# Kernel optimization log

Measured on AMD Instinct MI355X. Metric: run time of the kernel, lower is better.

## Reference

```python
import jax, jax.numpy as jnp
import numpy as np

N_NODES = 100000


def _gcn_layer(h_in, W, b, src, dst, n_nodes):
    """PyG GCNConv: out = D^{-1/2} (A + I) D^{-1/2} (h_in @ W) + b.
    src/dst already include self-loops. Messages flow src -> dst."""
    h = h_in @ W  # [N, C_out]
    ones = jnp.ones(dst.shape[0], dtype=h.dtype)
    deg = jax.ops.segment_sum(ones, dst, num_segments=n_nodes)  # in-degree incl. self-loops
    dinv = jnp.where(deg > 0, jax.lax.rsqrt(deg), 0.0)
    norm = dinv[src] * dinv[dst]  # [E]
    msg = norm[:, None] * h[src]  # gather + scale, [E, C_out]
    out = jax.ops.segment_sum(msg, dst, num_segments=n_nodes)
    return out + b


def setup_inputs() -> dict:
    key = jax.random.key(0)
    ks = jax.random.split(key, 4)
    d_in, d_hid = 64, 64
    n_edges = 1600000
    x = jax.random.normal(ks[0], (N_NODES, d_in), dtype=jnp.float32)
    edge_index = jax.random.randint(ks[1], (2, n_edges), 0, N_NODES, dtype=jnp.int64)
    W1 = jax.random.normal(ks[2], (d_in, d_hid), dtype=jnp.float32) * (1.0 / np.sqrt(d_in))
    b1 = jnp.zeros((d_hid,), dtype=jnp.float32)
    W2 = jax.random.normal(ks[3], (d_hid, d_hid), dtype=jnp.float32) * (1.0 / np.sqrt(d_hid))
    b2 = jnp.zeros((d_hid,), dtype=jnp.float32)
    return {"x": x, "edge_index": edge_index, "W1": W1, "b1": b1, "W2": W2, "b2": b2}


def reference(x, edge_index, W1, b1, W2, b2):
    n = x.shape[0]
    loop = jnp.arange(n, dtype=edge_index.dtype)
    src = jnp.concatenate([edge_index[0], loop])  # add self-loops once, reused by both layers
    dst = jnp.concatenate([edge_index[1], loop])
    h = jax.nn.relu(_gcn_layer(x, W1, b1, src, dst, n))
    h = jax.nn.relu(_gcn_layer(h, W2, b2, src, dst, n))
    return h
```

## Files before the change

kernel.cpp:

```cpp
#include <hip/hip_runtime.h>
#include <hip/hip_bf16.h>


#define NDIM 64
#define BSHIFT 9
#define BNODES (1 << BSHIFT)
#define BCAP 10240
#define CHUNK 4096
#define PHASES 13
#define PSHIFT 13

typedef float v2f __attribute__((ext_vector_type(2)));
typedef __attribute__((ext_vector_type(8))) short short8b;
typedef __attribute__((ext_vector_type(4))) float f32x4;

__device__ __forceinline__ unsigned f2bf_rne(float f) {
  unsigned u = __float_as_uint(f);
  return (u + 0x7fffu + ((u >> 16) & 1u)) >> 16;
}

__global__ void init_cursor_kernel(int* __restrict__ bcursor, int nbuck) {
  int b = blockIdx.x * 256 + threadIdx.x;
  if (b < nbuck) bcursor[b] = b * BCAP;
}

__global__ __launch_bounds__(256) void bin_scatter_kernel(
    const int* __restrict__ src, const int* __restrict__ dst,
    int* __restrict__ bcursor, unsigned* __restrict__ binned, int nedges) {
  __shared__ int lcnt[256], lbase[256], lcur[256], gbase[256], tscan[256];
  __shared__ int2 stage[CHUNK];
  int t = threadIdx.x;
  int i0 = blockIdx.x * CHUNK;
  int iend = i0 + CHUNK; if (iend > nedges) iend = nedges;
  lcnt[t] = 0;
  __syncthreads();
  for (int i = i0 + t; i < iend; i += 256)
    atomicAdd(&lcnt[dst[i] >> BSHIFT], 1);
  __syncthreads();
  tscan[t] = lcnt[t];
  __syncthreads();
  for (int off = 1; off < 256; off <<= 1) {
    int tv = (t >= off) ? tscan[t - off] : 0;
    __syncthreads();
    tscan[t] += tv;
    __syncthreads();
  }
  lbase[t] = tscan[t] - lcnt[t];
  lcur[t] = lbase[t];
  if (lcnt[t] > 0) gbase[t] = atomicAdd(&bcursor[t], lcnt[t]);
  __syncthreads();
  for (int i = i0 + t; i < iend; i += 256) {
    int s = src[i], d = dst[i];
    int p = atomicAdd(&lcur[d >> BSHIFT], 1);
    stage[p] = make_int2(s, d);
  }
  __syncthreads();
  int cnt = iend - i0;
  for (int i = t; i < cnt; i += 256) {
    int2 pr = stage[i];
    int b = pr.y >> BSHIFT;
    unsigned pk = (((unsigned)(pr.y & (BNODES - 1))) << 17) | (unsigned)pr.x;
    int idx = gbase[b] + (i - lbase[b]);
    if (idx < (b + 1) * BCAP) binned[idx] = pk;
  }
}

__global__ __launch_bounds__(256) void csr_build_kernel(
    const unsigned* __restrict__ binned, const int* __restrict__ bcursor,
    int* __restrict__ rowbeg, int* __restrict__ rowend,
    int* __restrict__ csr_src, float* __restrict__ dinv, int n) {
  __shared__ int deg[BNODES], rpl[BNODES], tscan[256];
  __shared__ int pcnt[BNODES * PHASES];
  int b = blockIdx.x, t = threadIdx.x;
  int node0 = b << BSHIFT;
  int ncnt = n - node0; if (ncnt > BNODES) ncnt = BNODES;
  int e0 = b * BCAP;
  int ecnt = bcursor[b] - e0;
  if (ecnt > BCAP) ecnt = BCAP;
  for (int i = t; i < BNODES * PHASES; i += 256) pcnt[i] = 0;
  __syncthreads();
  for (int i = t; i < ecnt; i += 256) {
    unsigned u = binned[e0 + i];
    atomicAdd(&pcnt[(u >> 17) * PHASES + ((u & 0x1FFFFu) >> PSHIFT)], 1);
  }
  __syncthreads();
  for (int i = t; i < BNODES; i += 256) {
    int s = 0;
#pragma unroll
    for (int p = 0; p < PHASES; ++p) {
      int c = pcnt[i * PHASES + p];
      pcnt[i * PHASES + p] = s;
      s += c;
    }
    deg[i] = s;
  }
  __syncthreads();
  int d0 = deg[2 * t], d1 = deg[2 * t + 1];
  int ps = d0 + d1;
  tscan[t] = ps;
  __syncthreads();
  for (int off = 1; off < 256; off <<= 1) {
    int tv = (t >= off) ? tscan[t - off] : 0;
    __syncthreads();
    tscan[t] += tv;
    __syncthreads();
  }
  int eb = tscan[t] - ps;
  rpl[2 * t] = eb;
  rpl[2 * t + 1] = eb + d0;
  __syncthreads();
  for (int i = t; i < ncnt; i += 256) {
    rowbeg[node0 + i] = e0 + rpl[i];
    rowend[node0 + i] = e0 + rpl[i] + deg[i];
    dinv[node0 + i] = rsqrtf((float)deg[i] + 1.0f);
  }
  __syncthreads();
  for (int i = t; i < ecnt; i += 256) {
    unsigned u = binned[e0 + i];
    int nd = u >> 17;
    int s = (int)(u & 0x1FFFFu);
    int pos = rpl[nd] + atomicAdd(&pcnt[nd * PHASES + (s >> PSHIFT)], 1);
    csr_src[e0 + pos] = s;
  }
}

template <bool BF16IN>
__global__ __launch_bounds__(256) void gemm_mfma_kernel(
    const void* __restrict__ Xin, const float* __restrict__ W,
    const float* __restrict__ dinv, ushort* __restrict__ hsb, int nrows) {
  __shared__ __attribute__((aligned(16))) ushort stage[4][16 * NDIM];
  const int tid = threadIdx.x;
  const int l = tid & 63;
  const int wv = tid >> 6;
  const int lrow = l & 15;
  const int kg = l >> 4;

  short8b Whi[4][2], Wlo[4][2];
#pragma unroll
  for (int ct = 0; ct < 4; ++ct) {
#pragma unroll
    for (int ks = 0; ks < 2; ++ks) {
      const int c = ct * 16 + lrow;
      const int k0 = ks * 32 + kg * 8;
#pragma unroll
      for (int i = 0; i < 8; ++i) {
        float w = W[(k0 + i) * NDIM + c];
        unsigned hb = f2bf_rne(w);
        float hf = __uint_as_float(hb << 16);
        Whi[ct][ks][i] = (short)hb;
        Wlo[ct][ks][i] = (short)f2bf_rne(w - hf);
      }
    }
  }

  const int tiles = (nrows + 15) >> 4;
  for (int tb = blockIdx.x * 4; tb < tiles; tb += gridDim.x * 4) {
    const int t = tb + wv;
    const int row0 = t << 4;
    const int r = row0 + lrow;
    short8b Ahi[2], Alo[2];
    if (BF16IN) {
      const uint4* Xb = (const uint4*)Xin;
#pragma unroll
      for (int ks = 0; ks < 2; ++ks) {
        uint4 q = make_uint4(0u, 0u, 0u, 0u);
        if (r < nrows) q = Xb[(size_t)r * 8 + ks * 4 + kg];
        union { uint4 u; short8b s; } cv; cv.u = q;
        Ahi[ks] = cv.s;
        Alo[ks] = cv.s;
      }
    } else {
      const float4* Xf = (const float4*)Xin;
#pragma unroll
      for (int ks = 0; ks < 2; ++ks) {
        float4 xa = make_float4(0.f, 0.f, 0.f, 0.f);
        float4 xb = make_float4(0.f, 0.f, 0.f, 0.f);
        if (r < nrows) {
          xa = Xf[(size_t)r * 16 + ks * 8 + kg * 2];
          xb = Xf[(size_t)r * 16 + ks * 8 + kg * 2 + 1];
        }
        float xs[8] = {xa.x, xa.y, xa.z, xa.w, xb.x, xb.y, xb.z, xb.w};
#pragma unroll
        for (int i = 0; i < 8; ++i) {
          unsigned hb = f2bf_rne(xs[i]);
          float hf = __uint_as_float(hb << 16);
          Ahi[ks][i] = (short)hb;
          Alo[ks][i] = (short)f2bf_rne(xs[i] - hf);
        }
      }
    }
    f32x4 acc[4];
#pragma unroll
    for (int ct = 0; ct < 4; ++ct) {
      f32x4 a = {0.f, 0.f, 0.f, 0.f};
#pragma unroll
      for (int ks = 0; ks < 2; ++ks) {
        a = __builtin_amdgcn_mfma_f32_16x16x32_bf16(Ahi[ks], Whi[ct][ks], a, 0, 0, 0);
        a = __builtin_amdgcn_mfma_f32_16x16x32_bf16(Ahi[ks], Wlo[ct][ks], a, 0, 0, 0);
        if (!BF16IN)
          a = __builtin_amdgcn_mfma_f32_16x16x32_bf16(Alo[ks], Whi[ct][ks], a, 0, 0, 0);
      }
      acc[ct] = a;
    }
#pragma unroll
    for (int q = 0; q < 4; ++q) {
      const int rr = row0 + kg * 4 + q;
      const float di = (rr < nrows) ? dinv[rr] : 0.f;
#pragma unroll
      for (int ct = 0; ct < 4; ++ct)
        stage[wv][(kg * 4 + q) * NDIM + ct * 16 + lrow] =
            (ushort)f2bf_rne(acc[ct][q] * di);
    }
    __syncthreads();
#pragma unroll
    for (int e = 0; e < 2; ++e) {
      const int idx = e * 64 + l;
      const int rw = idx >> 3;
      if (row0 + rw < nrows)
        ((uint4*)hsb)[(size_t)(row0 + rw) * 8 + (idx & 7)] =
            ((const uint4*)stage[wv])[idx];
    }
    __syncthreads();
  }
}

__device__ __forceinline__ void add8(v2f* acc, uint4 q) {
  v2f a0, a1, a2, a3;
  a0.x = __uint_as_float(q.x << 16); a0.y = __uint_as_float(q.x & 0xffff0000u);
  a1.x = __uint_as_float(q.y << 16); a1.y = __uint_as_float(q.y & 0xffff0000u);
  a2.x = __uint_as_float(q.z << 16); a2.y = __uint_as_float(q.z & 0xffff0000u);
  a3.x = __uint_as_float(q.w << 16); a3.y = __uint_as_float(q.w & 0xffff0000u);
  acc[0] += a0; acc[1] += a1; acc[2] += a2; acc[3] += a3;
}

template <bool BF16OUT>
__global__ __launch_bounds__(256) void agg_epi_kernel(
    const int* __restrict__ rowbeg, const int* __restrict__ rowend,
    const int* __restrict__ csr_src, const uint4* __restrict__ hsb4,
    const float* __restrict__ dinv, const float4* __restrict__ b4,
    void* __restrict__ outp, int n) {
  int node = blockIdx.x * 4 + (threadIdx.x >> 6);
  if (node >= n) return;
  int l = threadIdx.x & 63;
  int sub = l >> 3, g = l & 7;
  int beg = rowbeg[node], end = rowend[node];
  v2f acc[4];
#pragma unroll
  for (int i = 0; i < 4; ++i) acc[i] = (v2f)(0.f);
  for (int base = beg; base < end; base += 64) {
    int m = end - base; if (m > 64) m = 64;
    int sidx = (l < m) ? csr_src[base + l] : 0;
    int j = 0;
    for (; j + 16 <= m; j += 16) {
      int s0 = __shfl(sidx, j + sub);
      int s1 = __shfl(sidx, j + 8 + sub);
      uint4 q0 = hsb4[(size_t)s0 * 8 + g];
      uint4 q1 = hsb4[(size_t)s1 * 8 + g];
      add8(acc, q0);
      add8(acc, q1);
    }
    for (; j < m; j += 8) {
      int e = j + sub;
      int s = __shfl(sidx, e < m ? e : 0);
      uint4 q = hsb4[(size_t)s * 8 + g];
      if (e < m) add8(acc, q);
    }
  }
  if (sub == 0) add8(acc, hsb4[(size_t)node * 8 + g]);
  float a[8];
#pragma unroll
  for (int i = 0; i < 4; ++i) { a[2 * i] = acc[i].x; a[2 * i + 1] = acc[i].y; }
#pragma unroll
  for (int i = 0; i < 8; ++i) {
    a[i] += __shfl_xor(a[i], 8);
    a[i] += __shfl_xor(a[i], 16);
    a[i] += __shfl_xor(a[i], 32);
  }
  if (sub == 0) {
    float di = dinv[node];
    float4 bb0 = b4[2 * g], bb1 = b4[2 * g + 1];
    float o[8];
    o[0] = fmaxf(di * a[0] + bb0.x, 0.f);
    o[1] = fmaxf(di * a[1] + bb0.y, 0.f);
    o[2] = fmaxf(di * a[2] + bb0.z, 0.f);
    o[3] = fmaxf(di * a[3] + bb0.w, 0.f);
    o[4] = fmaxf(di * a[4] + bb1.x, 0.f);
    o[5] = fmaxf(di * a[5] + bb1.y, 0.f);
    o[6] = fmaxf(di * a[6] + bb1.z, 0.f);
    o[7] = fmaxf(di * a[7] + bb1.w, 0.f);
    if (BF16OUT) {
      uint4 wv;
      wv.x = f2bf_rne(o[0]) | (f2bf_rne(o[1]) << 16);
      wv.y = f2bf_rne(o[2]) | (f2bf_rne(o[3]) << 16);
      wv.z = f2bf_rne(o[4]) | (f2bf_rne(o[5]) << 16);
      wv.w = f2bf_rne(o[6]) | (f2bf_rne(o[7]) << 16);
      ((uint4*)outp)[(size_t)node * 8 + g] = wv;
    } else {
      float4 o0 = make_float4(o[0], o[1], o[2], o[3]);
      float4 o1 = make_float4(o[4], o[5], o[6], o[7]);
      ((float4*)outp)[(size_t)node * 16 + 2 * g] = o0;
      ((float4*)outp)[(size_t)node * 16 + 2 * g + 1] = o1;
    }
  }
}

extern "C" void kernel_launch(void* const* d_in, const int* in_sizes, int n_in,
                              void* d_out, int out_size, void* d_ws, size_t ws_size,
                              hipStream_t stream) {
  const float* x  = (const float*)d_in[0];
  const int* eidx = (const int*)d_in[1];
  const float* W1 = (const float*)d_in[2];
  const float* b1 = (const float*)d_in[3];
  const float* W2 = (const float*)d_in[4];
  const float* b2 = (const float*)d_in[5];
  float* out = (float*)d_out;

  const int N = in_sizes[0] / NDIM;
  const int E = in_sizes[1] / 2;
  const int* src = eidx;
  const int* dst = eidx + E;
  const int NV = N * NDIM;
  const int nbuck = (N + BNODES - 1) >> BSHIFT;
  const int nchunk = (E + CHUNK - 1) / CHUNK;

  auto al128 = [](size_t v) { return (v + 127) & ~(size_t)127; };
  char* w = (char*)d_ws;
  unsigned* binned = (unsigned*)w;  w += al128((size_t)nbuck * BCAP * 4);
  int*   csr_src = (int*)w;    w += al128((size_t)nbuck * BCAP * 4);
  int*   rowbeg  = (int*)w;    w += al128((size_t)N * 4);
  int*   rowend  = (int*)w;    w += al128((size_t)N * 4);
  float* dinv    = (float*)w;  w += al128((size_t)N * 4);
  int*   bcursor = (int*)w;    w += 2048;
  ushort* hsb = (ushort*)w;  w += al128((size_t)NV * 2);
  ushort* h2b = (ushort*)w;

  init_cursor_kernel<<<1, 256, 0, stream>>>(bcursor, nbuck);
  bin_scatter_kernel<<<nchunk, 256, 0, stream>>>(src, dst, bcursor, binned, E);
  csr_build_kernel<<<nbuck, 256, 0, stream>>>(binned, bcursor, rowbeg, rowend,
                                              csr_src, dinv, N);

  gemm_mfma_kernel<false><<<512, 256, 0, stream>>>(x, W1, dinv, hsb, N);
  agg_epi_kernel<true><<<(N + 3) / 4, 256, 0, stream>>>(
      rowbeg, rowend, csr_src, (const uint4*)hsb, dinv, (const float4*)b1, h2b, N);

  gemm_mfma_kernel<true><<<512, 256, 0, stream>>>(h2b, W2, dinv, hsb, N);
  agg_epi_kernel<false><<<(N + 3) / 4, 256, 0, stream>>>(
      rowbeg, rowend, csr_src, (const uint4*)hsb, dinv, (const float4*)b2, out, N);
}
```

Before: 245.8 us.

## Fuse all GCN stages into one persistent cooperative kernel with grid syncs

The seven separate launches (cursor init, binning, CSR build, two GEMMs, two aggregations) become a single cooperative persistent kernel. Each stage is a grid-stride device function, and grid.sync() separates the stages. Shared memory is a union of the per-stage layouts, and CHUNK is reduced to keep the LDS footprint low enough for 4 blocks per CU. This removes launch gaps and tail effects between kernels. In exchange, every stage runs at a fixed occupancy, register pressure is shared across all phases, and grid-wide barriers carry their own cost.

Measured after the change: 746.1 us. +203.5%, slower.

```diff
diff --git a/kernel.cpp b/kernel.cpp
--- a/kernel.cpp
+++ b/kernel.cpp
@@ -1,12 +1,15 @@
 #include <hip/hip_runtime.h>
+#include <hip/hip_cooperative_groups.h>
 #include <hip/hip_bf16.h>
+
+namespace cg = cooperative_groups;
 
 
 #define NDIM 64
 #define BSHIFT 9
 #define BNODES (1 << BSHIFT)
 #define BCAP 10240
-#define CHUNK 4096
+#define CHUNK 3072
 #define PHASES 13
 #define PSHIFT 13
 
@@ -14,121 +17,132 @@
 typedef __attribute__((ext_vector_type(8))) short short8b;
 typedef __attribute__((ext_vector_type(4))) float f32x4;
 
+struct BinSh {
+  int lcnt[256], lbase[256], lcur[256], gbase[256], tscan[256];
+  int2 stage[CHUNK];
+};
+struct CsrSh {
+  int deg[BNODES], rpl[BNODES], tscan[256];
+  int pcnt[BNODES * PHASES];
+};
+union SharedU {
+  BinSh bin;
+  CsrSh csr;
+  ushort gstage[4][16 * NDIM];
+};
+
 __device__ __forceinline__ unsigned f2bf_rne(float f) {
   unsigned u = __float_as_uint(f);
   return (u + 0x7fffu + ((u >> 16) & 1u)) >> 16;
 }
 
-__global__ void init_cursor_kernel(int* __restrict__ bcursor, int nbuck) {
-  int b = blockIdx.x * 256 + threadIdx.x;
-  if (b < nbuck) bcursor[b] = b * BCAP;
-}
-
-__global__ __launch_bounds__(256) void bin_scatter_kernel(
-    const int* __restrict__ src, const int* __restrict__ dst,
-    int* __restrict__ bcursor, unsigned* __restrict__ binned, int nedges) {
-  __shared__ int lcnt[256], lbase[256], lcur[256], gbase[256], tscan[256];
-  __shared__ int2 stage[CHUNK];
-  int t = threadIdx.x;
-  int i0 = blockIdx.x * CHUNK;
-  int iend = i0 + CHUNK; if (iend > nedges) iend = nedges;
-  lcnt[t] = 0;
-  __syncthreads();
-  for (int i = i0 + t; i < iend; i += 256)
-    atomicAdd(&lcnt[dst[i] >> BSHIFT], 1);
-  __syncthreads();
-  tscan[t] = lcnt[t];
-  __syncthreads();
-  for (int off = 1; off < 256; off <<= 1) {
-    int tv = (t >= off) ? tscan[t - off] : 0;
-    __syncthreads();
-    tscan[t] += tv;
-    __syncthreads();
-  }
-  lbase[t] = tscan[t] - lcnt[t];
-  lcur[t] = lbase[t];
-  if (lcnt[t] > 0) gbase[t] = atomicAdd(&bcursor[t], lcnt[t]);
-  __syncthreads();
-  for (int i = i0 + t; i < iend; i += 256) {
-    int s = src[i], d = dst[i];
-    int p = atomicAdd(&lcur[d >> BSHIFT], 1);
-    stage[p] = make_int2(s, d);
-  }
-  __syncthreads();
-  int cnt = iend - i0;
-  for (int i = t; i < cnt; i += 256) {
-    int2 pr = stage[i];
-    int b = pr.y >> BSHIFT;
-    unsigned pk = (((unsigned)(pr.y & (BNODES - 1))) << 17) | (unsigned)pr.x;
-    int idx = gbase[b] + (i - lbase[b]);
-    if (idx < (b + 1) * BCAP) binned[idx] = pk;
-  }
-}
-
-__global__ __launch_bounds__(256) void csr_build_kernel(
-    const unsigned* __restrict__ binned, const int* __restrict__ bcursor,
-    int* __restrict__ rowbeg, int* __restrict__ rowend,
-    int* __restrict__ csr_src, float* __restrict__ dinv, int n) {
-  __shared__ int deg[BNODES], rpl[BNODES], tscan[256];
-  __shared__ int pcnt[BNODES * PHASES];
-  int b = blockIdx.x, t = threadIdx.x;
-  int node0 = b << BSHIFT;
-  int ncnt = n - node0; if (ncnt > BNODES) ncnt = BNODES;
-  int e0 = b * BCAP;
-  int ecnt = bcursor[b] - e0;
-  if (ecnt > BCAP) ecnt = BCAP;
-  for (int i = t; i < BNODES * PHASES; i += 256) pcnt[i] = 0;
-  __syncthreads();
-  for (int i = t; i < ecnt; i += 256) {
-    unsigned u = binned[e0 + i];
-    atomicAdd(&pcnt[(u >> 17) * PHASES + ((u & 0x1FFFFu) >> PSHIFT)], 1);
-  }
-  __syncthreads();
-  for (int i = t; i < BNODES; i += 256) {
-    int s = 0;
-#pragma unroll
-    for (int p = 0; p < PHASES; ++p) {
-      int c = pcnt[i * PHASES + p];
-      pcnt[i * PHASES + p] = s;
-      s += c;
-    }
-    deg[i] = s;
-  }
-  __syncthreads();
-  int d0 = deg[2 * t], d1 = deg[2 * t + 1];
-  int ps = d0 + d1;
-  tscan[t] = ps;
-  __syncthreads();
-  for (int off = 1; off < 256; off <<= 1) {
-    int tv = (t >= off) ? tscan[t - off] : 0;
-    __syncthreads();
-    tscan[t] += tv;
-    __syncthreads();
-  }
-  int eb = tscan[t] - ps;
-  rpl[2 * t] = eb;
-  rpl[2 * t + 1] = eb + d0;
-  __syncthreads();
-  for (int i = t; i < ncnt; i += 256) {
-    rowbeg[node0 + i] = e0 + rpl[i];
-    rowend[node0 + i] = e0 + rpl[i] + deg[i];
-    dinv[node0 + i] = rsqrtf((float)deg[i] + 1.0f);
-  }
-  __syncthreads();
-  for (int i = t; i < ecnt; i += 256) {
-    unsigned u = binned[e0 + i];
-    int nd = u >> 17;
-    int s = (int)(u & 0x1FFFFu);
-    int pos = rpl[nd] + atomicAdd(&pcnt[nd * PHASES + (s >> PSHIFT)], 1);
-    csr_src[e0 + pos] = s;
+__device__ void phase_bin(const int* __restrict__ src, const int* __restrict__ dst,
+                          int* __restrict__ bcursor, unsigned* __restrict__ binned,
+                          int nedges, int nchunk, SharedU& sh) {
+  const int t = threadIdx.x;
+  for (int c = blockIdx.x; c < nchunk; c += gridDim.x) {
+    int i0 = c * CHUNK;
+    int iend = i0 + CHUNK; if (iend > nedges) iend = nedges;
+    sh.bin.lcnt[t] = 0;
+    __syncthreads();
+    for (int i = i0 + t; i < iend; i += 256)
+      atomicAdd(&sh.bin.lcnt[dst[i] >> BSHIFT], 1);
+    __syncthreads();
+    sh.bin.tscan[t] = sh.bin.lcnt[t];
+    __syncthreads();
+    for (int off = 1; off < 256; off <<= 1) {
+      int tv = (t >= off) ? sh.bin.tscan[t - off] : 0;
+      __syncthreads();
+      sh.bin.tscan[t] += tv;
+      __syncthreads();
+    }
+    sh.bin.lbase[t] = sh.bin.tscan[t] - sh.bin.lcnt[t];
+    sh.bin.lcur[t] = sh.bin.lbase[t];
+    if (sh.bin.lcnt[t] > 0) sh.bin.gbase[t] = atomicAdd(&bcursor[t], sh.bin.lcnt[t]);
+    __syncthreads();
+    for (int i = i0 + t; i < iend; i += 256) {
+      int s = src[i], d = dst[i];
+      int p = atomicAdd(&sh.bin.lcur[d >> BSHIFT], 1);
+      sh.bin.stage[p] = make_int2(s, d);
+    }
+    __syncthreads();
+    int cnt = iend - i0;
+    for (int i = t; i < cnt; i += 256) {
+      int2 pr = sh.bin.stage[i];
+      int b = pr.y >> BSHIFT;
+      unsigned pk = (((unsigned)(pr.y & (BNODES - 1))) << 17) | (unsigned)pr.x;
+      int idx = sh.bin.gbase[b] + (i - sh.bin.lbase[b]);
+      if (idx < (b + 1) * BCAP) binned[idx] = pk;
+    }
+    __syncthreads();
+  }
+}
+
+__device__ void phase_csr(const unsigned* __restrict__ binned,
+                          const int* __restrict__ bcursor,
+                          int* __restrict__ rowbeg, int* __restrict__ rowend,
+                          int* __restrict__ csr_src, float* __restrict__ dinv,
+                          int n, int nbuck, SharedU& sh) {
+  const int t = threadIdx.x;
+  for (int b = blockIdx.x; b < nbuck; b += gridDim.x) {
+    int node0 = b << BSHIFT;
+    int ncnt = n - node0; if (ncnt > BNODES) ncnt = BNODES;
+    int e0 = b * BCAP;
+    int ecnt = bcursor[b] - e0;
+    if (ecnt > BCAP) ecnt = BCAP;
+    for (int i = t; i < BNODES * PHASES; i += 256) sh.csr.pcnt[i] = 0;
+    __syncthreads();
+    for (int i = t; i < ecnt; i += 256) {
+      unsigned u = binned[e0 + i];
+      atomicAdd(&sh.csr.pcnt[(u >> 17) * PHASES + ((u & 0x1FFFFu) >> PSHIFT)], 1);
+    }
+    __syncthreads();
+    for (int i = t; i < BNODES; i += 256) {
+      int s = 0;
+#pragma unroll
+      for (int p = 0; p < PHASES; ++p) {
+        int c = sh.csr.pcnt[i * PHASES + p];
+        sh.csr.pcnt[i * PHASES + p] = s;
+        s += c;
+      }
+      sh.csr.deg[i] = s;
+    }
+    __syncthreads();
+    int d0 = sh.csr.deg[2 * t], d1 = sh.csr.deg[2 * t + 1];
+    int ps = d0 + d1;
+    sh.csr.tscan[t] = ps;
+    __syncthreads();
+    for (int off = 1; off < 256; off <<= 1) {
+      int tv = (t >= off) ? sh.csr.tscan[t - off] : 0;
+      __syncthreads();
+      sh.csr.tscan[t] += tv;
+      __syncthreads();
+    }
+    int eb = sh.csr.tscan[t] - ps;
+    sh.csr.rpl[2 * t] = eb;
+    sh.csr.rpl[2 * t + 1] = eb + d0;
+    __syncthreads();
+    for (int i = t; i < ncnt; i += 256) {
+      rowbeg[node0 + i] = e0 + sh.csr.rpl[i];
+      rowend[node0 + i] = e0 + sh.csr.rpl[i] + sh.csr.deg[i];
+      dinv[node0 + i] = rsqrtf((float)sh.csr.deg[i] + 1.0f);
+    }
+    __syncthreads();
+    for (int i = t; i < ecnt; i += 256) {
+      unsigned u = binned[e0 + i];
+      int nd = u >> 17;
+      int s = (int)(u & 0x1FFFFu);
+      int pos = sh.csr.rpl[nd] + atomicAdd(&sh.csr.pcnt[nd * PHASES + (s >> PSHIFT)], 1);
+      csr_src[e0 + pos] = s;
+    }
+    __syncthreads();
   }
 }
 
 template <bool BF16IN>
-__global__ __launch_bounds__(256) void gemm_mfma_kernel(
-    const void* __restrict__ Xin, const float* __restrict__ W,
-    const float* __restrict__ dinv, ushort* __restrict__ hsb, int nrows) {
-  __shared__ __attribute__((aligned(16))) ushort stage[4][16 * NDIM];
+__device__ void phase_gemm(const void* __restrict__ Xin, const float* __restrict__ W,
+                           const float* __restrict__ dinv, ushort* __restrict__ hsb,
+                           int nrows, SharedU& sh) {
   const int tid = threadIdx.x;
   const int l = tid & 63;
   const int wv = tid >> 6;
@@ -208,7 +222,7 @@
       const float di = (rr < nrows) ? dinv[rr] : 0.f;
 #pragma unroll
       for (int ct = 0; ct < 4; ++ct)
-        stage[wv][(kg * 4 + q) * NDIM + ct * 16 + lrow] =
+        sh.gstage[wv][(kg * 4 + q) * NDIM + ct * 16 + lrow] =
             (ushort)f2bf_rne(acc[ct][q] * di);
     }
     __syncthreads();
@@ -218,7 +232,7 @@
       const int rw = idx >> 3;
       if (row0 + rw < nrows)
         ((uint4*)hsb)[(size_t)(row0 + rw) * 8 + (idx & 7)] =
-            ((const uint4*)stage[wv])[idx];
+            ((const uint4*)sh.gstage[wv])[idx];
     }
     __syncthreads();
   }
@@ -234,74 +248,106 @@
 }
 
 template <bool BF16OUT>
-__global__ __launch_bounds__(256) void agg_epi_kernel(
-    const int* __restrict__ rowbeg, const int* __restrict__ rowend,
-    const int* __restrict__ csr_src, const uint4* __restrict__ hsb4,
-    const float* __restrict__ dinv, const float4* __restrict__ b4,
-    void* __restrict__ outp, int n) {
-  int node = blockIdx.x * 4 + (threadIdx.x >> 6);
-  if (node >= n) return;
-  int l = threadIdx.x & 63;
-  int sub = l >> 3, g = l & 7;
-  int beg = rowbeg[node], end = rowend[node];
-  v2f acc[4];
-#pragma unroll
-  for (int i = 0; i < 4; ++i) acc[i] = (v2f)(0.f);
-  for (int base = beg; base < end; base += 64) {
-    int m = end - base; if (m > 64) m = 64;
-    int sidx = (l < m) ? csr_src[base + l] : 0;
-    int j = 0;
-    for (; j + 16 <= m; j += 16) {
-      int s0 = __shfl(sidx, j + sub);
-      int s1 = __shfl(sidx, j + 8 + sub);
-      uint4 q0 = hsb4[(size_t)s0 * 8 + g];
-      uint4 q1 = hsb4[(size_t)s1 * 8 + g];
-      add8(acc, q0);
-      add8(acc, q1);
-    }
-    for (; j < m; j += 8) {
-      int e = j + sub;
-      int s = __shfl(sidx, e < m ? e : 0);
-      uint4 q = hsb4[(size_t)s * 8 + g];
-      if (e < m) add8(acc, q);
-    }
-  }
-  if (sub == 0) add8(acc, hsb4[(size_t)node * 8 + g]);
-  float a[8];
-#pragma unroll
-  for (int i = 0; i < 4; ++i) { a[2 * i] = acc[i].x; a[2 * i + 1] = acc[i].y; }
-#pragma unroll
-  for (int i = 0; i < 8; ++i) {
-    a[i] += __shfl_xor(a[i], 8);
-    a[i] += __shfl_xor(a[i], 16);
-    a[i] += __shfl_xor(a[i], 32);
-  }
-  if (sub == 0) {
-    float di = dinv[node];
-    float4 bb0 = b4[2 * g], bb1 = b4[2 * g + 1];
-    float o[8];
-    o[0] = fmaxf(di * a[0] + bb0.x, 0.f);
-    o[1] = fmaxf(di * a[1] + bb0.y, 0.f);
-    o[2] = fmaxf(di * a[2] + bb0.z, 0.f);
-    o[3] = fmaxf(di * a[3] + bb0.w, 0.f);
-    o[4] = fmaxf(di * a[4] + bb1.x, 0.f);
-    o[5] = fmaxf(di * a[5] + bb1.y, 0.f);
-    o[6] = fmaxf(di * a[6] + bb1.z, 0.f);
-    o[7] = fmaxf(di * a[7] + bb1.w, 0.f);
-    if (BF16OUT) {
-      uint4 wv;
-      wv.x = f2bf_rne(o[0]) | (f2bf_rne(o[1]) << 16);
-      wv.y = f2bf_rne(o[2]) | (f2bf_rne(o[3]) << 16);
-      wv.z = f2bf_rne(o[4]) | (f2bf_rne(o[5]) << 16);
-      wv.w = f2bf_rne(o[6]) | (f2bf_rne(o[7]) << 16);
-      ((uint4*)outp)[(size_t)node * 8 + g] = wv;
-    } else {
-      float4 o0 = make_float4(o[0], o[1], o[2], o[3]);
-      float4 o1 = make_float4(o[4], o[5], o[6], o[7]);
-      ((float4*)outp)[(size_t)node * 16 + 2 * g] = o0;
-      ((float4*)outp)[(size_t)node * 16 + 2 * g + 1] = o1;
-    }
-  }
+__device__ void phase_agg(const int* __restrict__ rowbeg, const int* __restrict__ rowend,
+                          const int* __restrict__ csr_src, const uint4* __restrict__ hsb4,
+                          const float* __restrict__ dinv, const float4* __restrict__ b4,
+                          void* __restrict__ outp, int n) {
+  const int wv = threadIdx.x >> 6;
+  const int l = threadIdx.x & 63;
+  const int sub = l >> 3, g = l & 7;
+  const int ngrp = (n + 3) >> 2;
+  for (int gi = blockIdx.x; gi < ngrp; gi += gridDim.x) {
+    int node = gi * 4 + wv;
+    if (node < n) {
+      int beg = rowbeg[node], end = rowend[node];
+      v2f acc[4];
+#pragma unroll
+      for (int i = 0; i < 4; ++i) acc[i] = (v2f)(0.f);
+      for (int base = beg; base < end; base += 64) {
+        int m = end - base; if (m > 64) m = 64;
+        int sidx = (l < m) ? csr_src[base + l] : 0;
+        int j = 0;
+        for (; j + 16 <= m; j += 16) {
+          int s0 = __shfl(sidx, j + sub);
+          int s1 = __shfl(sidx, j + 8 + sub);
+          uint4 q0 = hsb4[(size_t)s0 * 8 + g];
+          uint4 q1 = hsb4[(size_t)s1 * 8 + g];
+          add8(acc, q0);
+          add8(acc, q1);
+        }
+        for (; j < m; j += 8) {
+          int e = j + sub;
+          int s = __shfl(sidx, e < m ? e : 0);
+          uint4 q = hsb4[(size_t)s * 8 + g];
+          if (e < m) add8(acc, q);
+        }
+      }
+      if (sub == 0) add8(acc, hsb4[(size_t)node * 8 + g]);
+      float a[8];
+#pragma unroll
+      for (int i = 0; i < 4; ++i) { a[2 * i] = acc[i].x; a[2 * i + 1] = acc[i].y; }
+#pragma unroll
+      for (int i = 0; i < 8; ++i) {
+        a[i] += __shfl_xor(a[i], 8);
+        a[i] += __shfl_xor(a[i], 16);
+        a[i] += __shfl_xor(a[i], 32);
+      }
+      if (sub == 0) {
+        float di = dinv[node];
+        float4 bb0 = b4[2 * g], bb1 = b4[2 * g + 1];
+        float o[8];
+        o[0] = fmaxf(di * a[0] + bb0.x, 0.f);
+        o[1] = fmaxf(di * a[1] + bb0.y, 0.f);
+        o[2] = fmaxf(di * a[2] + bb0.z, 0.f);
+        o[3] = fmaxf(di * a[3] + bb0.w, 0.f);
+        o[4] = fmaxf(di * a[4] + bb1.x, 0.f);
+        o[5] = fmaxf(di * a[5] + bb1.y, 0.f);
+        o[6] = fmaxf(di * a[6] + bb1.z, 0.f);
+        o[7] = fmaxf(di * a[7] + bb1.w, 0.f);
+        if (BF16OUT) {
+          uint4 wvv;
+          wvv.x = f2bf_rne(o[0]) | (f2bf_rne(o[1]) << 16);
+          wvv.y = f2bf_rne(o[2]) | (f2bf_rne(o[3]) << 16);
+          wvv.z = f2bf_rne(o[4]) | (f2bf_rne(o[5]) << 16);
+          wvv.w = f2bf_rne(o[6]) | (f2bf_rne(o[7]) << 16);
+          ((uint4*)outp)[(size_t)node * 8 + g] = wvv;
+        } else {
+          float4 o0 = make_float4(o[0], o[1], o[2], o[3]);
+          float4 o1 = make_float4(o[4], o[5], o[6], o[7]);
+          ((float4*)outp)[(size_t)node * 16 + 2 * g] = o0;
+          ((float4*)outp)[(size_t)node * 16 + 2 * g + 1] = o1;
+        }
+      }
+    }
+  }
+}
+
+__global__ __launch_bounds__(256, 4) void fused_kernel(
+    const int* src, const int* dst, int* bcursor, unsigned* binned,
+    int* rowbeg, int* rowend, int* csr_src, float* dinv,
+    const float* x, const float* W1, const float* b1,
+    const float* W2, const float* b2,
+    ushort* hsb, ushort* h2b, float* out,
+    int n, int nedges, int nbuck, int nchunk) {
+  __shared__ __align__(16) SharedU sh;
+  cg::grid_group grid = cg::this_grid();
+
+  for (int b = blockIdx.x * 256 + threadIdx.x; b < nbuck; b += gridDim.x * 256)
+    bcursor[b] = b * BCAP;
+  grid.sync();
+  phase_bin(src, dst, bcursor, binned, nedges, nchunk, sh);
+  grid.sync();
+  phase_csr(binned, bcursor, rowbeg, rowend, csr_src, dinv, n, nbuck, sh);
+  grid.sync();
+  phase_gemm<false>((const void*)x, W1, dinv, hsb, n, sh);
+  grid.sync();
+  phase_agg<true>(rowbeg, rowend, csr_src, (const uint4*)hsb, dinv,
+                  (const float4*)b1, (void*)h2b, n);
+  grid.sync();
+  phase_gemm<true>((const void*)h2b, W2, dinv, hsb, n, sh);
+  grid.sync();
+  phase_agg<false>(rowbeg, rowend, csr_src, (const uint4*)hsb, dinv,
+                   (const float4*)b2, (void*)out, n);
 }
 
 extern "C" void kernel_launch(void* const* d_in, const int* in_sizes, int n_in,
@@ -334,16 +380,33 @@
   ushort* hsb = (ushort*)w;  w += al128((size_t)NV * 2);
   ushort* h2b = (ushort*)w;
 
-  init_cursor_kernel<<<1, 256, 0, stream>>>(bcursor, nbuck);
-  bin_scatter_kernel<<<nchunk, 256, 0, stream>>>(src, dst, bcursor, binned, E);
-  csr_build_kernel<<<nbuck, 256, 0, stream>>>(binned, bcursor, rowbeg, rowend,
-                                              csr_src, dinv, N);
-
-  gemm_mfma_kernel<false><<<512, 256, 0, stream>>>(x, W1, dinv, hsb, N);
-  agg_epi_kernel<true><<<(N + 3) / 4, 256, 0, stream>>>(
-      rowbeg, rowend, csr_src, (const uint4*)hsb, dinv, (const float4*)b1, h2b, N);
-
-  gemm_mfma_kernel<true><<<512, 256, 0, stream>>>(h2b, W2, dinv, hsb, N);
-  agg_epi_kernel<false><<<(N + 3) / 4, 256, 0, stream>>>(
-      rowbeg, rowend, csr_src, (const uint4*)hsb, dinv, (const float4*)b2, out, N);
-}
+  static int nblk = 0;
+  if (nblk == 0) {
+    int perCU = 0;
+    hipOccupancyMaxActiveBlocksPerMultiprocessor(
+        &perCU, reinterpret_cast<const void*>(fused_kernel), 256, 0);
+    if (perCU < 1) perCU = 1;
+    hipDeviceProp_t prop{};
+    int ncu = 256;
+    if (hipGetDeviceProperties(&prop, 0) == hipSuccess &&
+        prop.multiProcessorCount > 0)
+      ncu = prop.multiProcessorCount;
+    nblk = perCU * ncu;
+  }
+
+  const int* p_src = src;  const int* p_dst = dst;
+  int* p_bcursor = bcursor; unsigned* p_binned = binned;
+  int* p_rowbeg = rowbeg;  int* p_rowend = rowend;
+  int* p_csr = csr_src;    float* p_dinv = dinv;
+  const float* p_x = x;    const float* p_W1 = W1; const float* p_b1 = b1;
+  const float* p_W2 = W2;  const float* p_b2 = b2;
+  ushort* p_hsb = hsb;     ushort* p_h2b = h2b;    float* p_out = out;
+  int p_n = N, p_e = E, p_nbuck = nbuck, p_nchunk = nchunk;
+  void* args[] = {&p_src, &p_dst, &p_bcursor, &p_binned,
+                  &p_rowbeg, &p_rowend, &p_csr, &p_dinv,
+                  &p_x, &p_W1, &p_b1, &p_W2, &p_b2,
+                  &p_hsb, &p_h2b, &p_out,
+                  &p_n, &p_e, &p_nbuck, &p_nchunk};
+  hipLaunchCooperativeKernel(reinterpret_cast<const void*>(fused_kernel),
+                             dim3(nblk), dim3(256), args, 0, stream);
+}
```

## Fuse CSR build with layer-1 GEMM and layer-1 aggregation with layer-2 GEMM

Applied to the files above, without the earlier changes.

Merges the CSR-building kernel with the first feature transform, so each bucket block also computes X·W1 for its own 512 nodes once dinv is known. Merges the layer-1 aggregation epilogue with the layer-2 GEMM using 1024-thread blocks that aggregate 16 nodes into shared memory and then run MFMA on them, so the intermediate bf16 activation never goes to global memory. This removes two kernel launches and one global round trip. In exchange, the GEMM in the CSR kernel runs on only nbuck blocks, W2 is reconverted in every block, and only 4 of 16 waves do the MFMA work.

Result: slower. 259.9 us (+5.7%).

```diff
diff --git a/kernel.cpp b/kernel.cpp
--- a/kernel.cpp
+++ b/kernel.cpp
@@ -65,76 +65,80 @@
   }
 }
 
-__global__ __launch_bounds__(256) void csr_build_kernel(
+struct CsrSh {
+  int deg[BNODES], rpl[BNODES], tscan[256];
+  int pcnt[BNODES * PHASES];
+};
+union CsrGemmSh {
+  CsrSh c;
+  ushort g[4][16 * NDIM];
+};
+
+__global__ __launch_bounds__(256) void csr_gemm1_kernel(
     const unsigned* __restrict__ binned, const int* __restrict__ bcursor,
     int* __restrict__ rowbeg, int* __restrict__ rowend,
-    int* __restrict__ csr_src, float* __restrict__ dinv, int n) {
-  __shared__ int deg[BNODES], rpl[BNODES], tscan[256];
-  __shared__ int pcnt[BNODES * PHASES];
-  int b = blockIdx.x, t = threadIdx.x;
-  int node0 = b << BSHIFT;
+    int* __restrict__ csr_src, float* __restrict__ dinv,
+    const float* __restrict__ X, const float* __restrict__ W,
+    ushort* __restrict__ hsb, int n) {
+  __shared__ __align__(16) CsrGemmSh sh;
+  const int b = blockIdx.x, t = threadIdx.x;
+  const int node0 = b << BSHIFT;
   int ncnt = n - node0; if (ncnt > BNODES) ncnt = BNODES;
-  int e0 = b * BCAP;
+  const int e0 = b * BCAP;
   int ecnt = bcursor[b] - e0;
   if (ecnt > BCAP) ecnt = BCAP;
-  for (int i = t; i < BNODES * PHASES; i += 256) pcnt[i] = 0;
+
+  for (int i = t; i < BNODES * PHASES; i += 256) sh.c.pcnt[i] = 0;
   __syncthreads();
   for (int i = t; i < ecnt; i += 256) {
     unsigned u = binned[e0 + i];
-    atomicAdd(&pcnt[(u >> 17) * PHASES + ((u & 0x1FFFFu) >> PSHIFT)], 1);
+    atomicAdd(&sh.c.pcnt[(u >> 17) * PHASES + ((u & 0x1FFFFu) >> PSHIFT)], 1);
   }
   __syncthreads();
   for (int i = t; i < BNODES; i += 256) {
     int s = 0;
 #pragma unroll
     for (int p = 0; p < PHASES; ++p) {
-      int c = pcnt[i * PHASES + p];
-      pcnt[i * PHASES + p] = s;
+      int c = sh.c.pcnt[i * PHASES + p];
+      sh.c.pcnt[i * PHASES + p] = s;
       s += c;
     }
-    deg[i] = s;
-  }
-  __syncthreads();
-  int d0 = deg[2 * t], d1 = deg[2 * t + 1];
+    sh.c.deg[i] = s;
+  }
+  __syncthreads();
+  int d0 = sh.c.deg[2 * t], d1 = sh.c.deg[2 * t + 1];
   int ps = d0 + d1;
-  tscan[t] = ps;
+  sh.c.tscan[t] = ps;
   __syncthreads();
   for (int off = 1; off < 256; off <<= 1) {
-    int tv = (t >= off) ? tscan[t - off] : 0;
+    int tv = (t >= off) ? sh.c.tscan[t - off] : 0;
     __syncthreads();
-    tscan[t] += tv;
+    sh.c.tscan[t] += tv;
     __syncthreads();
   }
-  int eb = tscan[t] - ps;
-  rpl[2 * t] = eb;
-  rpl[2 * t + 1] = eb + d0;
+  int eb = sh.c.tscan[t] - ps;
+  sh.c.rpl[2 * t] = eb;
+  sh.c.rpl[2 * t + 1] = eb + d0;
   __syncthreads();
   for (int i = t; i < ncnt; i += 256) {
-    rowbeg[node0 + i] = e0 + rpl[i];
-    rowend[node0 + i] = e0 + rpl[i] + deg[i];
-    dinv[node0 + i] = rsqrtf((float)deg[i] + 1.0f);
+    rowbeg[node0 + i] = e0 + sh.c.rpl[i];
+    rowend[node0 + i] = e0 + sh.c.rpl[i] + sh.c.deg[i];
+    dinv[node0 + i] = rsqrtf((float)sh.c.deg[i] + 1.0f);
   }
   __syncthreads();
   for (int i = t; i < ecnt; i += 256) {
     unsigned u = binned[e0 + i];
     int nd = u >> 17;
     int s = (int)(u & 0x1FFFFu);
-    int pos = rpl[nd] + atomicAdd(&pcnt[nd * PHASES + (s >> PSHIFT)], 1);
+    int pos = sh.c.rpl[nd] + atomicAdd(&sh.c.pcnt[nd * PHASES + (s >> PSHIFT)], 1);
     csr_src[e0 + pos] = s;
   }
-}
-
-template <bool BF16IN>
-__global__ __launch_bounds__(256) void gemm_mfma_kernel(
-    const void* __restrict__ Xin, const float* __restrict__ W,
-    const float* __restrict__ dinv, ushort* __restrict__ hsb, int nrows) {
-  __shared__ __attribute__((aligned(16))) ushort stage[4][16 * NDIM];
-  const int tid = threadIdx.x;
-  const int l = tid & 63;
-  const int wv = tid >> 6;
+  __syncthreads();
+
+  const int l = t & 63;
+  const int wv = t >> 6;
   const int lrow = l & 15;
   const int kg = l >> 4;
-
   short8b Whi[4][2], Wlo[4][2];
 #pragma unroll
   for (int ct = 0; ct < 4; ++ct) {
@@ -152,41 +156,27 @@
       }
     }
   }
-
-  const int tiles = (nrows + 15) >> 4;
-  for (int tb = blockIdx.x * 4; tb < tiles; tb += gridDim.x * 4) {
-    const int t = tb + wv;
-    const int row0 = t << 4;
+  const int ntile = (ncnt + 15) >> 4;
+  for (int ti = wv; ti < ntile; ti += 4) {
+    const int row0 = node0 + (ti << 4);
     const int r = row0 + lrow;
     short8b Ahi[2], Alo[2];
-    if (BF16IN) {
-      const uint4* Xb = (const uint4*)Xin;
-#pragma unroll
-      for (int ks = 0; ks < 2; ++ks) {
-        uint4 q = make_uint4(0u, 0u, 0u, 0u);
-        if (r < nrows) q = Xb[(size_t)r * 8 + ks * 4 + kg];
-        union { uint4 u; short8b s; } cv; cv.u = q;
-        Ahi[ks] = cv.s;
-        Alo[ks] = cv.s;
-      }
-    } else {
-      const float4* Xf = (const float4*)Xin;
-#pragma unroll
-      for (int ks = 0; ks < 2; ++ks) {
-        float4 xa = make_float4(0.f, 0.f, 0.f, 0.f);
-        float4 xb = make_float4(0.f, 0.f, 0.f, 0.f);
-        if (r < nrows) {
-          xa = Xf[(size_t)r * 16 + ks * 8 + kg * 2];
-          xb = Xf[(size_t)r * 16 + ks * 8 + kg * 2 + 1];
-        }
-        float xs[8] = {xa.x, xa.y, xa.z, xa.w, xb.x, xb.y, xb.z, xb.w};
-#pragma unroll
-        for (int i = 0; i < 8; ++i) {
-          unsigned hb = f2bf_rne(xs[i]);
-          float hf = __uint_as_float(hb << 16);
-          Ahi[ks][i] = (short)hb;
-          Alo[ks][i] = (short)f2bf_rne(xs[i] - hf);
-        }
+    const float4* Xf = (const float4*)X;
+#pragma unroll
+    for (int ks = 0; ks < 2; ++ks) {
+      float4 xa = make_float4(0.f, 0.f, 0.f, 0.f);
+      float4 xb = make_float4(0.f, 0.f, 0.f, 0.f);
+      if (r < n) {
+        xa = Xf[(size_t)r * 16 + ks * 8 + kg * 2];
+        xb = Xf[(size_t)r * 16 + ks * 8 + kg * 2 + 1];
+      }
+      float xs[8] = {xa.x, xa.y, xa.z, xa.w, xb.x, xb.y, xb.z, xb.w};
+#pragma unroll
+      for (int i = 0; i < 8; ++i) {
+        unsigned hb = f2bf_rne(xs[i]);
+        float hf = __uint_as_float(hb << 16);
+        Ahi[ks][i] = (short)hb;
+        Alo[ks][i] = (short)f2bf_rne(xs[i] - hf);
       }
     }
     f32x4 acc[4];
@@ -197,30 +187,27 @@
       for (int ks = 0; ks < 2; ++ks) {
         a = __builtin_amdgcn_mfma_f32_16x16x32_bf16(Ahi[ks], Whi[ct][ks], a, 0, 0, 0);
         a = __builtin_amdgcn_mfma_f32_16x16x32_bf16(Ahi[ks], Wlo[ct][ks], a, 0, 0, 0);
-        if (!BF16IN)
-          a = __builtin_amdgcn_mfma_f32_16x16x32_bf16(Alo[ks], Whi[ct][ks], a, 0, 0, 0);
+        a = __builtin_amdgcn_mfma_f32_16x16x32_bf16(Alo[ks], Whi[ct][ks], a, 0, 0, 0);
       }
       acc[ct] = a;
     }
 #pragma unroll
     for (int q = 0; q < 4; ++q) {
       const int rr = row0 + kg * 4 + q;
-      const float di = (rr < nrows) ? dinv[rr] : 0.f;
+      const float di = (rr < n) ? dinv[rr] : 0.f;
 #pragma unroll
       for (int ct = 0; ct < 4; ++ct)
-        stage[wv][(kg * 4 + q) * NDIM + ct * 16 + lrow] =
+        sh.g[wv][(kg * 4 + q) * NDIM + ct * 16 + lrow] =
             (ushort)f2bf_rne(acc[ct][q] * di);
     }
-    __syncthreads();
 #pragma unroll
     for (int e = 0; e < 2; ++e) {
       const int idx = e * 64 + l;
       const int rw = idx >> 3;
-      if (row0 + rw < nrows)
+      if (row0 + rw < n)
         ((uint4*)hsb)[(size_t)(row0 + rw) * 8 + (idx & 7)] =
-            ((const uint4*)stage[wv])[idx];
-    }
-    __syncthreads();
+            ((const uint4*)sh.g[wv])[idx];
+    }
   }
 }
 
@@ -233,12 +220,121 @@
   acc[0] += a0; acc[1] += a1; acc[2] += a2; acc[3] += a3;
 }
 
-template <bool BF16OUT>
-__global__ __launch_bounds__(256) void agg_epi_kernel(
+__global__ __launch_bounds__(1024) void agg1_gemm2_kernel(
     const int* __restrict__ rowbeg, const int* __restrict__ rowend,
     const int* __restrict__ csr_src, const uint4* __restrict__ hsb4,
     const float* __restrict__ dinv, const float4* __restrict__ b4,
-    void* __restrict__ outp, int n) {
+    const float* __restrict__ W, ushort* __restrict__ hsb2, int n) {
+  __shared__ __align__(16) ushort h2s[16][NDIM + 8];
+  const int t = threadIdx.x;
+  const int wv = t >> 6;
+  const int l = t & 63;
+  const int sub = l >> 3, g = l & 7;
+  const int row0 = blockIdx.x * 16;
+  const int node = row0 + wv;
+
+  if (node < n) {
+    int beg = rowbeg[node], end = rowend[node];
+    v2f acc[4];
+#pragma unroll
+    for (int i = 0; i < 4; ++i) acc[i] = (v2f)(0.f);
+    for (int base = beg; base < end; base += 64) {
+      int m = end - base; if (m > 64) m = 64;
+      int sidx = (l < m) ? csr_src[base + l] : 0;
+      int j = 0;
+      for (; j + 16 <= m; j += 16) {
+        int s0 = __shfl(sidx, j + sub);
+        int s1 = __shfl(sidx, j + 8 + sub);
+        uint4 q0 = hsb4[(size_t)s0 * 8 + g];
+        uint4 q1 = hsb4[(size_t)s1 * 8 + g];
+        add8(acc, q0);
+        add8(acc, q1);
+      }
+      for (; j < m; j += 8) {
+        int e = j + sub;
+        int s = __shfl(sidx, e < m ? e : 0);
+        uint4 q = hsb4[(size_t)s * 8 + g];
+        if (e < m) add8(acc, q);
+      }
+    }
+    if (sub == 0) add8(acc, hsb4[(size_t)node * 8 + g]);
+    float a[8];
+#pragma unroll
+    for (int i = 0; i < 4; ++i) { a[2 * i] = acc[i].x; a[2 * i + 1] = acc[i].y; }
+#pragma unroll
+    for (int i = 0; i < 8; ++i) {
+      a[i] += __shfl_xor(a[i], 8);
+      a[i] += __shfl_xor(a[i], 16);
+      a[i] += __shfl_xor(a[i], 32);
+    }
+    if (sub == 0) {
+      float di = dinv[node];
+      float4 bb0 = b4[2 * g], bb1 = b4[2 * g + 1];
+      uint4 wvv;
+      wvv.x = f2bf_rne(fmaxf(di * a[0] + bb0.x, 0.f)) |
+              (f2bf_rne(fmaxf(di * a[1] + bb0.y, 0.f)) << 16);
+      wvv.y = f2bf_rne(fmaxf(di * a[2] + bb0.z, 0.f)) |
+              (f2bf_rne(fmaxf(di * a[3] + bb0.w, 0.f)) << 16);
+      wvv.z = f2bf_rne(fmaxf(di * a[4] + bb1.x, 0.f)) |
+              (f2bf_rne(fmaxf(di * a[5] + bb1.y, 0.f)) << 16);
+      wvv.w = f2bf_rne(fmaxf(di * a[6] + bb1.z, 0.f)) |
+              (f2bf_rne(fmaxf(di * a[7] + bb1.w, 0.f)) << 16);
+      *((uint4*)&h2s[wv][g * 8]) = wvv;
+    }
+  } else if (sub == 0) {
+    uint4 z = make_uint4(0u, 0u, 0u, 0u);
+    *((uint4*)&h2s[wv][g * 8]) = z;
+  }
+  __syncthreads();
+
+  const int lrow = l & 15, kg = l >> 4;
+  short8b Ahi[2], Whi[2], Wlo[2];
+  if (wv < 4) {
+    const int ct = wv;
+#pragma unroll
+    for (int ks = 0; ks < 2; ++ks) {
+      Ahi[ks] = *((const short8b*)&h2s[lrow][ks * 32 + kg * 8]);
+      const int c = ct * 16 + lrow;
+      const int k0 = ks * 32 + kg * 8;
+#pragma unroll
+      for (int i = 0; i < 8; ++i) {
+        float w = W[(k0 + i) * NDIM + c];
+        unsigned hb = f2bf_rne(w);
+        float hf = __uint_as_float(hb << 16);
+        Whi[ks][i] = (short)hb;
+        Wlo[ks][i] = (short)f2bf_rne(w - hf);
+      }
+    }
+  }
+  __syncthreads();
+  if (wv < 4) {
+    const int ct = wv;
+    f32x4 acc = {0.f, 0.f, 0.f, 0.f};
+    acc = __builtin_amdgcn_mfma_f32_16x16x32_bf16(Ahi[0], Whi[0], acc, 0, 0, 0);
+    acc = __builtin_amdgcn_mfma_f32_16x16x32_bf16(Ahi[0], Wlo[0], acc, 0, 0, 0);
+    acc = __builtin_amdgcn_mfma_f32_16x16x32_bf16(Ahi[1], Whi[1], acc, 0, 0, 0);
+    acc = __builtin_amdgcn_mfma_f32_16x16x32_bf16(Ahi[1], Wlo[1], acc, 0, 0, 0);
+#pragma unroll
+    for (int q = 0; q < 4; ++q) {
+      const int rr = row0 + kg * 4 + q;
+      const float di = (rr < n) ? dinv[rr] : 0.f;
+      h2s[kg * 4 + q][ct * 16 + lrow] = (ushort)f2bf_rne(acc[q] * di);
+    }
+  }
+  __syncthreads();
+  if (t < 128) {
+    const int rw = t >> 3, c8 = t & 7;
+    if (row0 + rw < n)
+      ((uint4*)hsb2)[(size_t)(row0 + rw) * 8 + c8] =
+          *((const uint4*)&h2s[rw][c8 * 8]);
+  }
+}
+
+__global__ __launch_bounds__(256) void agg2_kernel(
+    const int* __restrict__ rowbeg, const int* __restrict__ rowend,
+    const int* __restrict__ csr_src, const uint4* __restrict__ hsb4,
+    const float* __restrict__ dinv, const float4* __restrict__ b4,
+    float* __restrict__ outp, int n) {
   int node = blockIdx.x * 4 + (threadIdx.x >> 6);
   if (node >= n) return;
   int l = threadIdx.x & 63;
@@ -279,28 +375,17 @@
   if (sub == 0) {
     float di = dinv[node];
     float4 bb0 = b4[2 * g], bb1 = b4[2 * g + 1];
-    float o[8];
-    o[0] = fmaxf(di * a[0] + bb0.x, 0.f);
-    o[1] = fmaxf(di * a[1] + bb0.y, 0.f);
-    o[2] = fmaxf(di * a[2] + bb0.z, 0.f);
-    o[3] = fmaxf(di * a[3] + bb0.w, 0.f);
-    o[4] = fmaxf(di * a[4] + bb1.x, 0.f);
-    o[5] = fmaxf(di * a[5] + bb1.y, 0.f);
-    o[6] = fmaxf(di * a[6] + bb1.z, 0.f);
-    o[7] = fmaxf(di * a[7] + bb1.w, 0.f);
-    if (BF16OUT) {
-      uint4 wv;
-      wv.x = f2bf_rne(o[0]) | (f2bf_rne(o[1]) << 16);
-      wv.y = f2bf_rne(o[2]) | (f2bf_rne(o[3]) << 16);
-      wv.z = f2bf_rne(o[4]) | (f2bf_rne(o[5]) << 16);
-      wv.w = f2bf_rne(o[6]) | (f2bf_rne(o[7]) << 16);
-      ((uint4*)outp)[(size_t)node * 8 + g] = wv;
-    } else {
-      float4 o0 = make_float4(o[0], o[1], o[2], o[3]);
-      float4 o1 = make_float4(o[4], o[5], o[6], o[7]);
-      ((float4*)outp)[(size_t)node * 16 + 2 * g] = o0;
-      ((float4*)outp)[(size_t)node * 16 + 2 * g + 1] = o1;
-    }
+    float4 o0, o1;
+    o0.x = fmaxf(di * a[0] + bb0.x, 0.f);
+    o0.y = fmaxf(di * a[1] + bb0.y, 0.f);
+    o0.z = fmaxf(di * a[2] + bb0.z, 0.f);
+    o0.w = fmaxf(di * a[3] + bb0.w, 0.f);
+    o1.x = fmaxf(di * a[4] + bb1.x, 0.f);
+    o1.y = fmaxf(di * a[5] + bb1.y, 0.f);
+    o1.z = fmaxf(di * a[6] + bb1.z, 0.f);
+    o1.w = fmaxf(di * a[7] + bb1.w, 0.f);
+    ((float4*)outp)[(size_t)node * 16 + 2 * g] = o0;
+    ((float4*)outp)[(size_t)node * 16 + 2 * g + 1] = o1;
   }
 }
 
@@ -331,19 +416,17 @@
   int*   rowend  = (int*)w;    w += al128((size_t)N * 4);
   float* dinv    = (float*)w;  w += al128((size_t)N * 4);
   int*   bcursor = (int*)w;    w += 2048;
-  ushort* hsb = (ushort*)w;  w += al128((size_t)NV * 2);
-  ushort* h2b = (ushort*)w;
+  ushort* hsb  = (ushort*)w;  w += al128((size_t)NV * 2);
+  ushort* hsb2 = (ushort*)w;
 
   init_cursor_kernel<<<1, 256, 0, stream>>>(bcursor, nbuck);
   bin_scatter_kernel<<<nchunk, 256, 0, stream>>>(src, dst, bcursor, binned, E);
-  csr_build_kernel<<<nbuck, 256, 0, stream>>>(binned, bcursor, rowbeg, rowend,
-                                              csr_src, dinv, N);
-
-  gemm_mfma_kernel<false><<<512, 256, 0, stream>>>(x, W1, dinv, hsb, N);
-  agg_epi_kernel<true><<<(N + 3) / 4, 256, 0, stream>>>(
-      rowbeg, rowend, csr_src, (const uint4*)hsb, dinv, (const float4*)b1, h2b, N);
-
-  gemm_mfma_kernel<true><<<512, 256, 0, stream>>>(h2b, W2, dinv, hsb, N);
-  agg_epi_kernel<false><<<(N + 3) / 4, 256, 0, stream>>>(
-      rowbeg, rowend, csr_src, (const uint4*)hsb, dinv, (const float4*)b2, out, N);
-}
+  csr_gemm1_kernel<<<nbuck, 256, 0, stream>>>(binned, bcursor, rowbeg, rowend,
+                                              csr_src, dinv, x, W1, hsb, N);
+  agg1_gemm2_kernel<<<(N + 15) / 16, 1024, 0, stream>>>(
+      rowbeg, rowend, csr_src, (const uint4*)hsb, dinv, (const float4*)b1,
+      W2, hsb2, N);
+  agg2_kernel<<<(N + 3) / 4, 256, 0, stream>>>(
+      rowbeg, rowend, csr_src, (const uint4*)hsb2, dinv, (const float4*)b2,
+      out, N);
+}
```

## Map four nodes per wavefront in aggregation and replace cursor init with memset

Applied to the files above, without the earlier changes.

The aggregation kernel now gives each wavefront four destination nodes (16 lanes each) instead of one node per 64-lane wave. Each node's neighbors are processed two at a time in batches of 16, and the final reduction needs only one cross-lane shuffle step. This targets the waste of a full wave on low-degree nodes (about 17 edges on average), at the cost of divergence when degrees differ within a wave, since the loop runs to the maximum degree of the four nodes. The bucket cursor init kernel is replaced by a memset, with the bucket base offset now added inside the scatter kernel.

New measurement: 226.1 us. 8.0% less time.

```diff
diff --git a/kernel.cpp b/kernel.cpp
--- a/kernel.cpp
+++ b/kernel.cpp
@@ -17,11 +17,6 @@
 __device__ __forceinline__ unsigned f2bf_rne(float f) {
   unsigned u = __float_as_uint(f);
   return (u + 0x7fffu + ((u >> 16) & 1u)) >> 16;
-}
-
-__global__ void init_cursor_kernel(int* __restrict__ bcursor, int nbuck) {
-  int b = blockIdx.x * 256 + threadIdx.x;
-  if (b < nbuck) bcursor[b] = b * BCAP;
 }
 
 __global__ __launch_bounds__(256) void bin_scatter_kernel(
@@ -47,7 +42,7 @@
   }
   lbase[t] = tscan[t] - lcnt[t];
   lcur[t] = lbase[t];
-  if (lcnt[t] > 0) gbase[t] = atomicAdd(&bcursor[t], lcnt[t]);
+  if (lcnt[t] > 0) gbase[t] = t * BCAP + atomicAdd(&bcursor[t], lcnt[t]);
   __syncthreads();
   for (int i = i0 + t; i < iend; i += 256) {
     int s = src[i], d = dst[i];
@@ -75,7 +70,7 @@
   int node0 = b << BSHIFT;
   int ncnt = n - node0; if (ncnt > BNODES) ncnt = BNODES;
   int e0 = b * BCAP;
-  int ecnt = bcursor[b] - e0;
+  int ecnt = bcursor[b];
   if (ecnt > BCAP) ecnt = BCAP;
   for (int i = t; i < BNODES * PHASES; i += 256) pcnt[i] = 0;
   __syncthreads();
@@ -239,44 +234,45 @@
     const int* __restrict__ csr_src, const uint4* __restrict__ hsb4,
     const float* __restrict__ dinv, const float4* __restrict__ b4,
     void* __restrict__ outp, int n) {
-  int node = blockIdx.x * 4 + (threadIdx.x >> 6);
-  if (node >= n) return;
-  int l = threadIdx.x & 63;
-  int sub = l >> 3, g = l & 7;
-  int beg = rowbeg[node], end = rowend[node];
+  const int l = threadIdx.x & 63;
+  const int wv = threadIdx.x >> 6;
+  const int ql = l & 15;
+  const int sg = ql >> 3;
+  const int g = ql & 7;
+  const int node = blockIdx.x * 16 + wv * 4 + (l >> 4);
+  const bool alive = node < n;
+  const int nodec = alive ? node : 0;
+  int beg = rowbeg[nodec], end = rowend[nodec];
+  if (!alive) { beg = 0; end = 0; }
+  const int deg = end - beg;
+  int dmax = deg;
+  dmax = max(dmax, __shfl_xor(dmax, 16));
+  dmax = max(dmax, __shfl_xor(dmax, 32));
+
   v2f acc[4];
 #pragma unroll
   for (int i = 0; i < 4; ++i) acc[i] = (v2f)(0.f);
-  for (int base = beg; base < end; base += 64) {
-    int m = end - base; if (m > 64) m = 64;
-    int sidx = (l < m) ? csr_src[base + l] : 0;
-    int j = 0;
-    for (; j + 16 <= m; j += 16) {
-      int s0 = __shfl(sidx, j + sub);
-      int s1 = __shfl(sidx, j + 8 + sub);
-      uint4 q0 = hsb4[(size_t)s0 * 8 + g];
-      uint4 q1 = hsb4[(size_t)s1 * 8 + g];
-      add8(acc, q0);
-      add8(acc, q1);
-    }
-    for (; j < m; j += 8) {
-      int e = j + sub;
-      int s = __shfl(sidx, e < m ? e : 0);
+
+  for (int base = 0; base < dmax; base += 16) {
+    const int rem = deg - base;
+    int eidx = (ql < rem) ? csr_src[beg + base + ql] : 0;
+#pragma unroll
+    for (int j = 0; j < 16; j += 2) {
+      const int e = j + sg;
+      int s = __shfl(eidx, (l & 48) + e);
       uint4 q = hsb4[(size_t)s * 8 + g];
-      if (e < m) add8(acc, q);
-    }
-  }
-  if (sub == 0) add8(acc, hsb4[(size_t)node * 8 + g]);
+      if (e < rem) add8(acc, q);
+    }
+  }
+  if (sg == 0) add8(acc, hsb4[(size_t)nodec * 8 + g]);
+
   float a[8];
 #pragma unroll
   for (int i = 0; i < 4; ++i) { a[2 * i] = acc[i].x; a[2 * i + 1] = acc[i].y; }
 #pragma unroll
-  for (int i = 0; i < 8; ++i) {
-    a[i] += __shfl_xor(a[i], 8);
-    a[i] += __shfl_xor(a[i], 16);
-    a[i] += __shfl_xor(a[i], 32);
-  }
-  if (sub == 0) {
+  for (int i = 0; i < 8; ++i) a[i] += __shfl_xor(a[i], 8);
+
+  if (sg == 0 && alive) {
     float di = dinv[node];
     float4 bb0 = b4[2 * g], bb1 = b4[2 * g + 1];
     float o[8];
@@ -289,12 +285,12 @@
     o[6] = fmaxf(di * a[6] + bb1.z, 0.f);
     o[7] = fmaxf(di * a[7] + bb1.w, 0.f);
     if (BF16OUT) {
-      uint4 wv;
-      wv.x = f2bf_rne(o[0]) | (f2bf_rne(o[1]) << 16);
-      wv.y = f2bf_rne(o[2]) | (f2bf_rne(o[3]) << 16);
-      wv.z = f2bf_rne(o[4]) | (f2bf_rne(o[5]) << 16);
-      wv.w = f2bf_rne(o[6]) | (f2bf_rne(o[7]) << 16);
-      ((uint4*)outp)[(size_t)node * 8 + g] = wv;
+      uint4 wvv;
+      wvv.x = f2bf_rne(o[0]) | (f2bf_rne(o[1]) << 16);
+      wvv.y = f2bf_rne(o[2]) | (f2bf_rne(o[3]) << 16);
+      wvv.z = f2bf_rne(o[4]) | (f2bf_rne(o[5]) << 16);
+      wvv.w = f2bf_rne(o[6]) | (f2bf_rne(o[7]) << 16);
+      ((uint4*)outp)[(size_t)node * 8 + g] = wvv;
     } else {
       float4 o0 = make_float4(o[0], o[1], o[2], o[3]);
       float4 o1 = make_float4(o[4], o[5], o[6], o[7]);
@@ -334,16 +330,16 @@
   ushort* hsb = (ushort*)w;  w += al128((size_t)NV * 2);
   ushort* h2b = (ushort*)w;
 
-  init_cursor_kernel<<<1, 256, 0, stream>>>(bcursor, nbuck);
+  hipMemsetAsync(bcursor, 0, 1024, stream);
   bin_scatter_kernel<<<nchunk, 256, 0, stream>>>(src, dst, bcursor, binned, E);
   csr_build_kernel<<<nbuck, 256, 0, stream>>>(binned, bcursor, rowbeg, rowend,
                                               csr_src, dinv, N);
 
   gemm_mfma_kernel<false><<<512, 256, 0, stream>>>(x, W1, dinv, hsb, N);
-  agg_epi_kernel<true><<<(N + 3) / 4, 256, 0, stream>>>(
+  agg_epi_kernel<true><<<(N + 15) / 16, 256, 0, stream>>>(
       rowbeg, rowend, csr_src, (const uint4*)hsb, dinv, (const float4*)b1, h2b, N);
 
   gemm_mfma_kernel<true><<<512, 256, 0, stream>>>(h2b, W2, dinv, hsb, N);
-  agg_epi_kernel<false><<<(N + 3) / 4, 256, 0, stream>>>(
+  agg_epi_kernel<false><<<(N + 15) / 16, 256, 0, stream>>>(
       rowbeg, rowend, csr_src, (const uint4*)hsb, dinv, (const float4*)b2, out, N);
 }
```
